# Performance work log

Measured on AMD Instinct MI355X. Metric: run time of the kernel, lower is better.

Reference implementation:

```python
import jax, jax.numpy as jnp
import numpy as np

RHO = 10.0
TAU = 0.1


def setup_inputs() -> dict:
    key = jax.random.key(0)
    k1, k2 = jax.random.split(key)
    N, D, C = 8192, 512, 128
    embeddings = jax.random.normal(k1, (N, D), dtype=jnp.float32)
    classes = jax.random.randint(k2, (N,), 0, C, dtype=jnp.int64)
    return {"embeddings": embeddings, "classes": classes}


def reference(embeddings, classes):
    n = embeddings.shape[0]
    dt = embeddings.dtype

    # calculate_similarities_pt: cosine similarity (dot products of L2-normalized embeddings)
    norms = jnp.linalg.norm(embeddings, axis=1, keepdims=True)
    normed = embeddings / jnp.maximum(norms, jnp.asarray(1e-12, dt))
    dot_products = jnp.einsum("nd,md->nm", normed, normed)  # [N, N]

    # calculate_groups_pt: same-class mask (excluding self) and different-class mask
    eq = classes[:, None] == classes[None, :]
    eye = jnp.eye(n, dtype=bool)
    same_group = (eq & ~eye).astype(dt)       # [N, N]
    different_group = (~eq).astype(dt)        # [N, N]

    # diagonal gets factor -RHO -> strongly negative score, effectively masked out
    raw_scores = ((same_group + different_group) * (1.0 + RHO) - RHO) * dot_products / TAU
    max_raw_score = jnp.max(raw_scores, axis=1, keepdims=True)
    shifted_scores = jnp.exp(raw_scores - max_raw_score)

    shifted_positive_scores = same_group * shifted_scores
    sum_shifted_negative_scores = jnp.sum(different_group * shifted_scores, axis=1, keepdims=True)

    denom = shifted_positive_scores + sum_shifted_negative_scores
    # safe_division: 0 where denominator is 0
    ratio = jnp.where(denom > 0, shifted_positive_scores / jnp.where(denom > 0, denom, 1.0), 0.0)
    # safe_log: 0 where argument is 0 (masked by same_group anyway)
    log_ratio = jnp.where(ratio > 0, jnp.log(jnp.where(ratio > 0, ratio, 1.0)), 0.0)
    infonce_losses = -log_ratio * same_group

    num_pos = jnp.sum(same_group)
    loss = jnp.where(num_pos > 0, jnp.sum(infonce_losses) / jnp.where(num_pos > 0, num_pos, 1.0), 0.0)
    return loss
```

## Files before the change

### kernel.cpp

```cpp
#include <hip/hip_runtime.h>
#include <hip/hip_bf16.h>
#include <hip/hip_fp8.h>


constexpr int   D      = 512;
constexpr int   BT     = 128;
constexpr int   BK     = 64;
constexpr int   NSTEP  = D / BK;
constexpr float TAUINV = 10.0f;
constexpr float SHIFT  = 10.0f;

typedef __attribute__((ext_vector_type(4))) float f32x4;
typedef __attribute__((ext_vector_type(2))) long i64x2;
typedef unsigned char uchar;
typedef unsigned long ulong_t;

__device__ inline uchar f2fp8(float x) {
    __hip_fp8_e4m3 h(x);
    return (uchar)h.__x;
}

__device__ inline void gload_lds16(const uchar* g, void* l) {
    __builtin_amdgcn_global_load_lds(
        (const __attribute__((address_space(1))) void*)g,
        (__attribute__((address_space(3))) void*)l, 16, 0, 0);
}

__global__ void k_normalize(const float* __restrict__ emb,
                            const int* __restrict__ classes,
                            uchar* __restrict__ normed,
                            int* __restrict__ hist, int n) {
    if (blockIdx.x == 0) {
        __shared__ int h[128];
        if (threadIdx.x < 128) h[threadIdx.x] = 0;
        __syncthreads();
        for (int i = threadIdx.x; i < n; i += 256)
            atomicAdd(&h[classes[i] & 127], 1);
        __syncthreads();
        if (threadIdx.x < 128) hist[threadIdx.x] = h[threadIdx.x];
    }
    int row  = blockIdx.x * 4 + (threadIdx.x >> 6);
    int lane = threadIdx.x & 63;
    if (row >= n) return;
    const float4* src = (const float4*)(emb + (size_t)row * D);
    float4 a = src[lane * 2];
    float4 b = src[lane * 2 + 1];
    float ss = a.x*a.x + a.y*a.y + a.z*a.z + a.w*a.w
             + b.x*b.x + b.y*b.y + b.z*b.z + b.w*b.w;
#pragma unroll
    for (int m = 1; m < 64; m <<= 1) ss += __shfl_xor(ss, m, 64);
    float sc = 1.0f / fmaxf(sqrtf(ss), 1e-12f);
    union { uchar c[8]; ulong_t u; } o;
    o.c[0] = f2fp8(a.x * sc); o.c[1] = f2fp8(a.y * sc);
    o.c[2] = f2fp8(a.z * sc); o.c[3] = f2fp8(a.w * sc);
    o.c[4] = f2fp8(b.x * sc); o.c[5] = f2fp8(b.y * sc);
    o.c[6] = f2fp8(b.z * sc); o.c[7] = f2fp8(b.w * sc);
    int j8   = lane & 7;
    int doff = (lane >> 3) * 64 + (j8 & 3) * 16 + (j8 >> 2) * 8;
    *(ulong_t*)&normed[(size_t)row * D + doff] = o.u;
}

__global__ __launch_bounds__(256, 3) void k_zgemm(
    const uchar* __restrict__ normed, const int* __restrict__ classes,
    float* __restrict__ Zpart, int n, int nb, int npairs) {
    __shared__ char ring[3][16384];
    __shared__ int clsrow[BT], clscol[BT];

    const int tid  = threadIdx.x;
    const int lane = tid & 63;
    const int w    = tid >> 6;
    const int wm   = w >> 1, wn = w & 1;
    const int l15  = lane & 15, l4 = lane >> 4;
    const size_t QS = (size_t)64 * n;

    int q8 = npairs >> 3, r8 = npairs & 7;
    int xcd = blockIdx.x & 7, off = blockIdx.x >> 3;
    int orig = (xcd < r8 ? xcd * (q8 + 1) : r8 * (q8 + 1) + (xcd - r8) * q8) + off;

    const int sgrid = nb >> 3;
    int idx = orig, si = 0;
    for (;;) { int rc = 36 + (sgrid - 1 - si) * 64; if (idx < rc) break; idx -= rc; ++si; }
    int bi, bj;
    if (idx < 36) { int u = 0, rem = 8; while (idx >= rem) { idx -= rem; ++u; --rem; }
                    bi = si * 8 + u; bj = si * 8 + u + idx; }
    else { idx -= 36; int sj = si + 1 + (idx >> 6); int v = idx & 63;
           bi = si * 8 + (v >> 3); bj = sj * 8 + (v & 7); }
    const int row0 = bi * BT, c0 = bj * BT;
    const bool diagblk = (bi == bj);

    if (tid < BT) clsrow[tid] = classes[row0 + tid];
    else          clscol[tid - BT] = classes[c0 + tid - BT];
    int crow[16];
#pragma unroll
    for (int t = 0; t < 16; ++t)
        crow[t] = classes[row0 + wm * 64 + (t >> 2) * 16 + l4 * 4 + (t & 3)];

    const int src16 = (lane & 3) ^ ((lane >> 3) & 3);
    size_t gA[2], gB[2]; int lo[2];
#pragma unroll
    for (int it = 0; it < 2; ++it) {
        int chunk = w * 2 + it;
        int row   = chunk * 16 + (lane >> 2);
        gA[it] = (size_t)(row0 + row) * D + src16 * 16;
        gB[it] = (size_t)(c0   + row) * D + src16 * 16;
        lo[it] = chunk * 1024;
    }
    char* ringb = &ring[0][0];

    auto STAGE = [&](int sbo, int kk) {
#pragma unroll
        for (int it = 0; it < 2; ++it) {
            gload_lds16(normed + gA[it] + kk, ringb + sbo + lo[it]);
            gload_lds16(normed + gB[it] + kk, ringb + sbo + 8192 + lo[it]);
        }
    };

    f32x4 acc[4][4];
#pragma unroll
    for (int a = 0; a < 4; ++a)
#pragma unroll
        for (int b = 0; b < 4; ++b) acc[a][b] = (f32x4){0.f, 0.f, 0.f, 0.f};

    STAGE(0, 0);
    STAGE(16384, BK);
    __builtin_amdgcn_sched_barrier(0);
    asm volatile("s_waitcnt vmcnt(4) lgkmcnt(0)" ::: "memory");
    __builtin_amdgcn_s_barrier();
    __builtin_amdgcn_sched_barrier(0);

    const int rsw = (l15 >> 1) & 3;

#pragma unroll
    for (int kt = 0; kt < NSTEP; ++kt) {
        const int cur = kt % 3;
        if (kt + 2 < NSTEP) STAGE(((kt + 2) % 3) * 16384, (kt + 2) * BK);
        const char* la = ringb + cur * 16384;
        const char* lb = la + 8192;
        i64x2 af[4], bfr[4];
#pragma unroll
        for (int mf = 0; mf < 4; ++mf) {
            int ra = wm * 64 + mf * 16 + l15;
            af[mf] = *(const i64x2*)(la + ra * 64 + ((l4 ^ rsw) << 4));
        }
#pragma unroll
        for (int nf = 0; nf < 4; ++nf) {
            int rb = wn * 64 + nf * 16 + l15;
            bfr[nf] = *(const i64x2*)(lb + rb * 64 + ((l4 ^ rsw) << 4));
        }
        __builtin_amdgcn_s_setprio(1);
#pragma unroll
        for (int mf = 0; mf < 4; ++mf)
#pragma unroll
            for (int nf = 0; nf < 4; ++nf) {
                acc[mf][nf] = __builtin_amdgcn_mfma_f32_16x16x32_fp8_fp8(
                    af[mf][0], bfr[nf][0], acc[mf][nf], 0, 0, 0);
                acc[mf][nf] = __builtin_amdgcn_mfma_f32_16x16x32_fp8_fp8(
                    af[mf][1], bfr[nf][1], acc[mf][nf], 0, 0, 0);
            }
        __builtin_amdgcn_s_setprio(0);
        __builtin_amdgcn_sched_barrier(0);
        if (kt + 2 < NSTEP)       asm volatile("s_waitcnt vmcnt(4)" ::: "memory");
        else if (kt + 2 == NSTEP) asm volatile("s_waitcnt vmcnt(0)" ::: "memory");
        if (kt + 1 < NSTEP) {
            __builtin_amdgcn_s_barrier();
            __builtin_amdgcn_sched_barrier(0);
        }
    }
    __syncthreads();

    float cqz[4] = {0,0,0,0}, cqn[4] = {0,0,0,0}, cqp[4] = {0,0,0,0};
    float* redr = (float*)ringb;
    float* redc = (float*)(ringb + 16384);

#pragma unroll
    for (int mf = 0; mf < 4; ++mf) {
#pragma unroll
        for (int r = 0; r < 4; ++r) {
            int rr = wm * 64 + mf * 16 + l4 * 4 + r;
            int rg = row0 + rr;
            int cr = crow[mf * 4 + r];
            float z = 0.f, ns = 0.f, p1 = 0.f;
#pragma unroll
            for (int nf = 0; nf < 4; ++nf) {
                int cc = wn * 64 + nf * 16 + l15;
                float t = fmaf(acc[mf][nf][r], TAUINV, -SHIFT);
                float e = __expf(t);
                bool same = (cr == clscol[cc]);
                bool dg   = (rg == c0 + cc);
                if (!same) { z += e; cqz[nf] += e; }
                else if (!dg) { ns += t; p1 += e; cqn[nf] += t; cqp[nf] += e; }
            }
#pragma unroll
            for (int m = 1; m < 16; m <<= 1) {
                z  += __shfl_xor(z,  m, 16);
                ns += __shfl_xor(ns, m, 16);
                p1 += __shfl_xor(p1, m, 16);
            }
            if (l15 == 0) {
                float* p = &redr[(wn * 128 + rr) * 3];
                p[0] = z; p[1] = ns; p[2] = p1;
            }
        }
    }
    if (!diagblk) {
#pragma unroll
        for (int nf = 0; nf < 4; ++nf) {
            float z = cqz[nf], nsv = cqn[nf], p = cqp[nf];
            z += __shfl_xor(z, 16, 64);  z += __shfl_xor(z, 32, 64);
            nsv += __shfl_xor(nsv, 16, 64); nsv += __shfl_xor(nsv, 32, 64);
            p += __shfl_xor(p, 16, 64);  p += __shfl_xor(p, 32, 64);
            if (l4 == 0) {
                float* pp = &redc[(wm * 128 + wn * 64 + nf * 16 + l15) * 3];
                pp[0] = z; pp[1] = nsv; pp[2] = p;
            }
        }
    }
    __syncthreads();

    if (tid < BT) {
#pragma unroll
        for (int q = 0; q < 3; ++q)
            Zpart[q * QS + (size_t)bj * n + row0 + tid] =
                redr[(0 * 128 + tid) * 3 + q] + redr[(1 * 128 + tid) * 3 + q];
    } else if (!diagblk) {
        int cc = tid - BT;
#pragma unroll
        for (int q = 0; q < 3; ++q)
            Zpart[q * QS + (size_t)bi * n + c0 + cc] =
                redc[(0 * 128 + cc) * 3 + q] + redc[(1 * 128 + cc) * 3 + q];
    }
}

__global__ void k_rowterms(const float* __restrict__ Zpart,
                           const int* __restrict__ classes,
                           const int* __restrict__ hist,
                           float* __restrict__ rowloss,
                           float* __restrict__ rowcnt, int n) {
    int i = blockIdx.x * 256 + threadIdx.x;
    if (i >= n) return;
    const size_t QS = (size_t)64 * n;
    float z = 0.f, ns = 0.f, p1 = 0.f;
    for (int s = 0; s < 64; ++s) {
        size_t o = (size_t)s * n + i;
        z  += Zpart[o];
        ns += Zpart[QS + o];
        p1 += Zpart[2 * QS + o];
    }
    float c = (float)(hist[classes[i] & 127] - 1);
    rowloss[i] = -ns + c * logf(z) + p1 / z;
    rowcnt[i]  = c;
}

__global__ void k_final(const float* __restrict__ rowloss,
                        const float* __restrict__ rowcnt,
                        float* __restrict__ out, int n) {
    __shared__ float sl[1024];
    __shared__ float sc[1024];
    float l = 0.f, c = 0.f;
    for (int i = threadIdx.x; i < n; i += 1024) {
        l += rowloss[i];
        c += rowcnt[i];
    }
    sl[threadIdx.x] = l;
    sc[threadIdx.x] = c;
    __syncthreads();
    for (int s = 512; s > 0; s >>= 1) {
        if (threadIdx.x < s) {
            sl[threadIdx.x] += sl[threadIdx.x + s];
            sc[threadIdx.x] += sc[threadIdx.x + s];
        }
        __syncthreads();
    }
    if (threadIdx.x == 0)
        out[0] = (sc[0] > 0.f) ? sl[0] / sc[0] : 0.f;
}

extern "C" void kernel_launch(void* const* d_in, const int* in_sizes, int n_in,
                              void* d_out, int out_size, void* d_ws, size_t ws_size,
                              hipStream_t stream) {
    const float* emb     = (const float*)d_in[0];
    const int*   classes = (const int*)d_in[1];
    float*       out     = (float*)d_out;
    const int n  = in_sizes[1];
    const int nb = n / BT;
    const int npairs = nb * (nb + 1) / 2;

    uchar*  normed  = (uchar*)d_ws;
    float*  Zpart   = (float*)((char*)d_ws + (size_t)n * D);
    float*  rowloss = Zpart + (size_t)3 * 64 * n;
    float*  rowcnt  = rowloss + n;
    int*    hist    = (int*)(rowcnt + n);

    k_normalize<<<n / 4, 256, 0, stream>>>(emb, classes, normed, hist, n);
    k_zgemm<<<npairs, 256, 0, stream>>>(normed, classes, Zpart, n, nb, npairs);
    k_rowterms<<<(n + 255) / 256, 256, 0, stream>>>(Zpart, classes, hist, rowloss, rowcnt, n);
    k_final<<<1, 1024, 0, stream>>>(rowloss, rowcnt, out, n);
}
```

Baseline: 81.82 us.

## Switch similarity GEMM from fp8 e4m3 MFMA to int8 MFMA with symmetric quantization

```diff
diff --git a/kernel.cpp b/kernel.cpp
--- a/kernel.cpp
+++ b/kernel.cpp
@@ -1,24 +1,17 @@
 #include <hip/hip_runtime.h>
 #include <hip/hip_bf16.h>
-#include <hip/hip_fp8.h>
 
 
 constexpr int   D      = 512;
 constexpr int   BT     = 128;
 constexpr int   BK     = 64;
 constexpr int   NSTEP  = D / BK;
-constexpr float TAUINV = 10.0f;
 constexpr float SHIFT  = 10.0f;
-
-typedef __attribute__((ext_vector_type(4))) float f32x4;
-typedef __attribute__((ext_vector_type(2))) long i64x2;
+constexpr float QS2    = 10.0f / 16129.0f;
+
+typedef __attribute__((ext_vector_type(4))) int i32x4;
 typedef unsigned char uchar;
 typedef unsigned long ulong_t;
-
-__device__ inline uchar f2fp8(float x) {
-    __hip_fp8_e4m3 h(x);
-    return (uchar)h.__x;
-}
 
 __device__ inline void gload_lds16(const uchar* g, void* l) {
     __builtin_amdgcn_global_load_lds(
@@ -49,15 +42,16 @@
              + b.x*b.x + b.y*b.y + b.z*b.z + b.w*b.w;
 #pragma unroll
     for (int m = 1; m < 64; m <<= 1) ss += __shfl_xor(ss, m, 64);
-    float sc = 1.0f / fmaxf(sqrtf(ss), 1e-12f);
-    union { uchar c[8]; ulong_t u; } o;
-    o.c[0] = f2fp8(a.x * sc); o.c[1] = f2fp8(a.y * sc);
-    o.c[2] = f2fp8(a.z * sc); o.c[3] = f2fp8(a.w * sc);
-    o.c[4] = f2fp8(b.x * sc); o.c[5] = f2fp8(b.y * sc);
-    o.c[6] = f2fp8(b.z * sc); o.c[7] = f2fp8(b.w * sc);
-    int j8   = lane & 7;
-    int doff = (lane >> 3) * 64 + (j8 & 3) * 16 + (j8 >> 2) * 8;
-    *(ulong_t*)&normed[(size_t)row * D + doff] = o.u;
+    float sc = 127.0f / fmaxf(sqrtf(ss), 1e-12f);
+    union { signed char c[8]; ulong_t u; } o;
+    float v[8] = {a.x, a.y, a.z, a.w, b.x, b.y, b.z, b.w};
+#pragma unroll
+    for (int k = 0; k < 8; ++k) {
+        int q = (int)rintf(v[k] * sc);
+        q = q > 127 ? 127 : (q < -127 ? -127 : q);
+        o.c[k] = (signed char)q;
+    }
+    *(ulong_t*)&normed[(size_t)row * D + lane * 8] = o.u;
 }
 
 __global__ __launch_bounds__(256, 3) void k_zgemm(
@@ -115,11 +109,11 @@
         }
     };
 
-    f32x4 acc[4][4];
+    i32x4 acc[4][4];
 #pragma unroll
     for (int a = 0; a < 4; ++a)
 #pragma unroll
-        for (int b = 0; b < 4; ++b) acc[a][b] = (f32x4){0.f, 0.f, 0.f, 0.f};
+        for (int b = 0; b < 4; ++b) acc[a][b] = (i32x4){0, 0, 0, 0};
 
     STAGE(0, 0);
     STAGE(16384, BK);
@@ -136,27 +130,24 @@
         if (kt + 2 < NSTEP) STAGE(((kt + 2) % 3) * 16384, (kt + 2) * BK);
         const char* la = ringb + cur * 16384;
         const char* lb = la + 8192;
-        i64x2 af[4], bfr[4];
+        i32x4 af[4], bfr[4];
 #pragma unroll
         for (int mf = 0; mf < 4; ++mf) {
             int ra = wm * 64 + mf * 16 + l15;
-            af[mf] = *(const i64x2*)(la + ra * 64 + ((l4 ^ rsw) << 4));
+            af[mf] = *(const i32x4*)(la + ra * 64 + ((l4 ^ rsw) << 4));
         }
 #pragma unroll
         for (int nf = 0; nf < 4; ++nf) {
             int rb = wn * 64 + nf * 16 + l15;
-            bfr[nf] = *(const i64x2*)(lb + rb * 64 + ((l4 ^ rsw) << 4));
+            bfr[nf] = *(const i32x4*)(lb + rb * 64 + ((l4 ^ rsw) << 4));
         }
         __builtin_amdgcn_s_setprio(1);
 #pragma unroll
         for (int mf = 0; mf < 4; ++mf)
 #pragma unroll
-            for (int nf = 0; nf < 4; ++nf) {
-                acc[mf][nf] = __builtin_amdgcn_mfma_f32_16x16x32_fp8_fp8(
-                    af[mf][0], bfr[nf][0], acc[mf][nf], 0, 0, 0);
-                acc[mf][nf] = __builtin_amdgcn_mfma_f32_16x16x32_fp8_fp8(
-                    af[mf][1], bfr[nf][1], acc[mf][nf], 0, 0, 0);
-            }
+            for (int nf = 0; nf < 4; ++nf)
+                acc[mf][nf] = __builtin_amdgcn_mfma_i32_16x16x64_i8(
+                    af[mf], bfr[nf], acc[mf][nf], 0, 0, 0);
         __builtin_amdgcn_s_setprio(0);
         __builtin_amdgcn_sched_barrier(0);
         if (kt + 2 < NSTEP)       asm volatile("s_waitcnt vmcnt(4)" ::: "memory");
@@ -183,7 +174,7 @@
 #pragma unroll
             for (int nf = 0; nf < 4; ++nf) {
                 int cc = wn * 64 + nf * 16 + l15;
-                float t = fmaf(acc[mf][nf][r], TAUINV, -SHIFT);
+                float t = fmaf((float)acc[mf][nf][r], QS2, -SHIFT);
                 float e = __expf(t);
                 bool same = (cr == clscol[cc]);
                 bool dg   = (rg == c0 + cc);
```

Result: faster. 75.84 us (-7.3%).
